# Kernel tuning notes

Hardware: AMD Instinct MI355X
Metric: run time of the kernel (lower is better)

## Reference

```python
import jax, jax.numpy as jnp
import numpy as np

D_MODEL = 512
D_FFN = 2048
N_LAYERS = 6
VOCAB = 1000
D_STATE = 16
D_CONV = 4
D_INNER = 2 * D_MODEL  # expand=2
DT_RANK = 32           # ceil(d_model/16)
B, LT, LS = 2, 512, 512


def _pos_encoding(length, d_model):
    pos = np.arange(length, dtype=np.float32)[:, None]
    div = np.exp(np.arange(0, d_model, 2, dtype=np.float32) * (-np.log(10000.0) / d_model))
    pe = np.zeros((length, d_model), np.float32)
    pe[:, 0::2] = np.sin(pos * div)
    pe[:, 1::2] = np.cos(pos * div)
    return jnp.asarray(pe)


def _layer_norm(x, g, b, eps=1e-6):
    m = x.mean(-1, keepdims=True)
    v = ((x - m) ** 2).mean(-1, keepdims=True)
    return (x - m) * jax.lax.rsqrt(v + eps) * g + b


def _mamba(x, in_w, conv_w, conv_b, xproj_w, dt_w, dt_b, A_log, Dskip, out_w):
    # x: (b, l, d_model)
    b, l, _ = x.shape
    xz = x @ in_w.T                                   # (b, l, 2*d_inner)
    xc, z = jnp.split(xz, 2, axis=-1)
    # causal depthwise conv over time
    xt = jnp.transpose(xc, (0, 2, 1))                 # (b, d_inner, l)
    xt = jnp.pad(xt, ((0, 0), (0, 0), (D_CONV - 1, 0)))
    xt = jax.lax.conv_general_dilated(
        xt, conv_w, window_strides=(1,), padding='VALID',
        feature_group_count=D_INNER, dimension_numbers=('NCH', 'OIH', 'NCH'))
    xc = jax.nn.silu(jnp.transpose(xt, (0, 2, 1)) + conv_b)  # (b, l, d_inner)
    dbl = xc @ xproj_w.T                              # (b, l, dt_rank + 2*n)
    dt, Bm, Cm = jnp.split(dbl, [DT_RANK, DT_RANK + D_STATE], axis=-1)
    dt = jax.nn.softplus(dt @ dt_w.T + dt_b)          # (b, l, d_inner)
    A = -jnp.exp(A_log)                               # (d_inner, n)

    def step(h, xs):
        dt_t, B_t, C_t, u_t = xs                      # (b,d),(b,n),(b,n),(b,d)
        dA = jnp.exp(dt_t[..., None] * A)             # (b, d, n)
        h = dA * h + (dt_t * u_t)[..., None] * B_t[:, None, :]
        y = jnp.einsum('bdn,bn->bd', h, C_t)
        return h, y

    h0 = jnp.zeros((b, D_INNER, D_STATE), x.dtype)
    xs = (jnp.swapaxes(dt, 0, 1), jnp.swapaxes(Bm, 0, 1),
          jnp.swapaxes(Cm, 0, 1), jnp.swapaxes(xc, 0, 1))
    _, ys = jax.lax.scan(step, h0, xs)                # ys: (l, b, d_inner)
    y = jnp.swapaxes(ys, 0, 1) + xc * Dskip
    y = y * jax.nn.silu(z)
    return y @ out_w.T                                # (b, l, d_model)


def setup_inputs() -> dict:
    key = jax.random.key(0)
    ks = iter(jax.random.split(key, 40))

    def rn(shape, s=0.02):
        return jax.random.normal(next(ks), shape, jnp.float32) * s

    def mamba_params():
        return dict(
            in_w=rn((N_LAYERS, 2 * D_INNER, D_MODEL)),
            conv_w=rn((N_LAYERS, D_INNER, 1, D_CONV), 0.1),
            conv_b=rn((N_LAYERS, D_INNER)),
            xproj=rn((N_LAYERS, DT_RANK + 2 * D_STATE, D_INNER)),
            dtw=rn((N_LAYERS, D_INNER, DT_RANK)),
            dtb=rn((N_LAYERS, D_INNER)),
            Alog=jnp.log(jnp.broadcast_to(jnp.arange(1.0, D_STATE + 1.0, dtype=jnp.float32), (N_LAYERS, D_INNER, D_STATE))),
            D=jnp.ones((N_LAYERS, D_INNER), jnp.float32),
            outw=rn((N_LAYERS, D_MODEL, D_INNER)),
        )

    ps, pc = mamba_params(), mamba_params()
    inp = {
        'src': jax.random.normal(next(ks), (B, LS, D_MODEL), jnp.float32),
        'tgt': jax.random.randint(next(ks), (B, LT), 0, VOCAB),
        'emb': rn((VOCAB, D_MODEL)),
        'in_w_s': ps['in_w'], 'conv_w_s': ps['conv_w'], 'conv_b_s': ps['conv_b'],
        'xproj_s': ps['xproj'], 'dtw_s': ps['dtw'], 'dtb_s': ps['dtb'],
        'Alog_s': ps['Alog'], 'D_s': ps['D'], 'outw_s': ps['outw'],
        'in_w_c': pc['in_w'], 'conv_w_c': pc['conv_w'], 'conv_b_c': pc['conv_b'],
        'xproj_c': pc['xproj'], 'dtw_c': pc['dtw'], 'dtb_c': pc['dtb'],
        'Alog_c': pc['Alog'], 'D_c': pc['D'], 'outw_c': pc['outw'],
        'ffn_w1': rn((N_LAYERS, D_FFN, D_MODEL)),
        'ffn_b1': jnp.zeros((N_LAYERS, D_FFN), jnp.float32),
        'ffn_w2': rn((N_LAYERS, D_MODEL, D_FFN)),
        'ffn_b2': jnp.zeros((N_LAYERS, D_MODEL), jnp.float32),
        'ln_g': jnp.ones((N_LAYERS, 3, D_MODEL), jnp.float32),
        'ln_b': jnp.zeros((N_LAYERS, 3, D_MODEL), jnp.float32),
        'fin_g': jnp.ones((D_MODEL,), jnp.float32),
        'fin_b': jnp.zeros((D_MODEL,), jnp.float32),
    }
    return inp


def reference(src, tgt, emb, in_w_s, conv_w_s, conv_b_s, xproj_s, dtw_s, dtb_s,
              Alog_s, D_s, outw_s, in_w_c, conv_w_c, conv_b_c, xproj_c, dtw_c,
              dtb_c, Alog_c, D_c, outw_c, ffn_w1, ffn_b1, ffn_w2, ffn_b2,
              ln_g, ln_b, fin_g, fin_b):
    # NormalizedEmbedding + sinusoidal positional encoding
    x = emb[tgt] * jnp.sqrt(jnp.asarray(D_MODEL, jnp.float32))
    x = x + _pos_encoding(LT, D_MODEL)[None]
    for i in range(N_LAYERS):
        # self mamba (post-norm, normalize_before=False)
        t2 = _mamba(x, in_w_s[i], conv_w_s[i], conv_b_s[i], xproj_s[i],
                    dtw_s[i], dtb_s[i], Alog_s[i], D_s[i], outw_s[i])
        x = _layer_norm(x + t2, ln_g[i, 0], ln_b[i, 0])
        # cross mamba over concat([memory, tgt]) then take last LT steps
        cat = jnp.concatenate([src, x], axis=1)
        t2 = _mamba(cat, in_w_c[i], conv_w_c[i], conv_b_c[i], xproj_c[i],
                    dtw_c[i], dtb_c[i], Alog_c[i], D_c[i], outw_c[i])[:, -LT:]
        x = _layer_norm(x + t2, ln_g[i, 1], ln_b[i, 1])
        # positionwise FFN
        h = jax.nn.relu(x @ ffn_w1[i].T + ffn_b1[i]) @ ffn_w2[i].T + ffn_b2[i]
        x = _layer_norm(x + h, ln_g[i, 2], ln_b[i, 2])
    return _layer_norm(x, fin_g, fin_b)
```

## Files before the change

kernel.cpp:

```cpp
#include <hip/hip_runtime.h>
#include <math.h>

#define DMODEL 512
#define DINNER 1024
#define DSTATE 16
#define DTRANK 32
#define NLAYERS 6
#define BB 2
#define LT 512
#define LS 512

typedef __attribute__((ext_vector_type(8))) short bf16x8;
typedef __attribute__((ext_vector_type(8))) unsigned short u16x8;
typedef __attribute__((ext_vector_type(4))) float f32x4;

__device__ __forceinline__ unsigned short f2bf(float f) {
  unsigned u = __float_as_uint(f);
  u += 0x7fffu + ((u >> 16) & 1u);
  return (unsigned short)(u >> 16);
}
__device__ __forceinline__ float bf2f(unsigned short u) {
  return __uint_as_float((unsigned)u << 16);
}

template<int EPI>
__device__ __forceinline__ float epi_apply(float acc, float b) {
  if (EPI == 1) { float v = acc + b; return v > 0.f ? v : 0.f; }
  if (EPI == 2) { return acc + b; }
  if (EPI == 3) { float v = acc + b; return fmaxf(v, 0.f) + log1pf(__expf(-fabsf(v))); }
  return acc;
}

__global__ __launch_bounds__(256) void cvt_all_kernel(
    const float* __restrict__ i0, const float* __restrict__ i1,
    const float* __restrict__ i2, const float* __restrict__ i3,
    const float* __restrict__ i4, const float* __restrict__ i5,
    const float* __restrict__ i6, const float* __restrict__ i7,
    const float* __restrict__ i8, const float* __restrict__ i9,
    unsigned short* __restrict__ outbase) {
  int i = blockIdx.x * 256 + threadIdx.x;
  if (i >= 8159232) return;
  const float* in; int off;
  if      (i < 1572864) { in = i0; off = i; }
  else if (i < 3145728) { in = i1; off = i - 1572864; }
  else if (i < 3244032) { in = i2; off = i - 3145728; }
  else if (i < 3342336) { in = i3; off = i - 3244032; }
  else if (i < 3391488) { in = i4; off = i - 3342336; }
  else if (i < 3440640) { in = i5; off = i - 3391488; }
  else if (i < 4227072) { in = i6; off = i - 3440640; }
  else if (i < 5013504) { in = i7; off = i - 4227072; }
  else if (i < 6586368) { in = i8; off = i - 5013504; }
  else                  { in = i9; off = i - 6586368; }
  float4 a = ((const float4*)in)[off];
  ushort4 o = make_ushort4(f2bf(a.x), f2bf(a.y), f2bf(a.z), f2bf(a.w));
  *(ushort4*)&outbase[(size_t)i * 4] = o;
}

__global__ __launch_bounds__(256) void embed_kernel(const int* __restrict__ tgt,
    const float* __restrict__ emb, float* __restrict__ X,
    unsigned short* __restrict__ Xb) {
  int i = blockIdx.x * 256 + threadIdx.x;
  int d = i & (DMODEL - 1);
  int bt = i >> 9;
  int t = bt & (LT - 1);
  int tok = tgt[bt];
  float div = __expf((float)(d & ~1) * (-9.210340371976184f / (float)DMODEL));
  float ang = (float)t * div;
  float pe = (d & 1) ? cosf(ang) : sinf(ang);
  float v = emb[(size_t)tok * DMODEL + d] * 22.627416997969522f + pe;
  X[i] = v;
  Xb[i] = f2bf(v);
}

__global__ __launch_bounds__(256) void catsrc_kernel(const float* __restrict__ src,
    unsigned short* __restrict__ CATb) {
  int i = blockIdx.x * 256 + threadIdx.x;
  int c8 = (i & 63) * 8;
  int r = i >> 6;
  int b = r >> 9, l = r & 511;
  const float* s = src + ((size_t)b * 512 + l) * DMODEL + c8;
  float4 a = *(const float4*)s;
  float4 bq = *(const float4*)(s + 4);
  u16x8 o;
  o[0] = f2bf(a.x); o[1] = f2bf(a.y); o[2] = f2bf(a.z); o[3] = f2bf(a.w);
  o[4] = f2bf(bq.x); o[5] = f2bf(bq.y); o[6] = f2bf(bq.z); o[7] = f2bf(bq.w);
  *(u16x8*)&CATb[((size_t)b * 1024 + l) * DMODEL + c8] = o;
}

template<int BK, int EPI, bool SPLIT, bool OUTB>
__global__ __launch_bounds__(256) void mgemmA(
    const unsigned short* __restrict__ A, const unsigned short* __restrict__ Bw,
    const float* __restrict__ bias, float* __restrict__ C,
    unsigned short* __restrict__ Cb, int M, int N, int K, int lda) {
  constexpr int PAD = BK + 8;
  constexpr int CHA = BK / 32;
  constexpr int CHB = BK / 16;
  __shared__ __align__(16) unsigned short As[64 * PAD];
  __shared__ __align__(16) unsigned short Bs[128 * PAD];
  const int tid = threadIdx.x;
  const int bn = blockIdx.x * 128;
  const int bm = blockIdx.y * 64;
  const int lane = tid & 63;
  const int w = tid >> 6;
  const int wr = (w >> 1) * 32;
  const int wc = (w & 1) * 64;
  const int l15 = lane & 15;
  const int l4 = lane >> 4;
  const int koff = l4 * 8;
  int kcnt = K, kbeg = 0;
  if (SPLIT) { kcnt = K / (int)gridDim.z; kbeg = blockIdx.z * kcnt; }
  const int nt = kcnt / BK;
  f32x4 acc[2][4] = {};

  int arow_[CHA], ak8_[CHA];
  const unsigned short* Ap[CHA];
#pragma unroll
  for (int i = 0; i < CHA; ++i) {
    int f = tid + 256 * i;
    arow_[i] = f / (BK / 8);
    ak8_[i] = (f % (BK / 8)) * 8;
    Ap[i] = A + (size_t)(bm + arow_[i]) * lda + kbeg + ak8_[i];
  }
  int brow_[CHB], bk8_[CHB];
  const unsigned short* Bp[CHB];
#pragma unroll
  for (int i = 0; i < CHB; ++i) {
    int f = tid + 256 * i;
    brow_[i] = f / (BK / 8);
    bk8_[i] = (f % (BK / 8)) * 8;
    Bp[i] = Bw + (size_t)(bn + brow_[i]) * K + kbeg + bk8_[i];
  }

  u16x8 av[CHA], bv[CHB];
#pragma unroll
  for (int i = 0; i < CHA; ++i) av[i] = *(const u16x8*)Ap[i];
#pragma unroll
  for (int i = 0; i < CHB; ++i) bv[i] = *(const u16x8*)Bp[i];

  for (int t = 0; t < nt; ++t) {
    __syncthreads();
#pragma unroll
    for (int i = 0; i < CHA; ++i) *(u16x8*)&As[arow_[i] * PAD + ak8_[i]] = av[i];
#pragma unroll
    for (int i = 0; i < CHB; ++i) *(u16x8*)&Bs[brow_[i] * PAD + bk8_[i]] = bv[i];
    if (t + 1 < nt) {
      int ko = (t + 1) * BK;
#pragma unroll
      for (int i = 0; i < CHA; ++i) av[i] = *(const u16x8*)(Ap[i] + ko);
#pragma unroll
      for (int i = 0; i < CHB; ++i) bv[i] = *(const u16x8*)(Bp[i] + ko);
    }
    __syncthreads();
#pragma unroll
    for (int kk = 0; kk < BK / 32; ++kk) {
      bf16x8 afr[2], bfr[4];
#pragma unroll
      for (int i = 0; i < 2; ++i)
        afr[i] = *(const bf16x8*)&As[(wr + i * 16 + l15) * PAD + kk * 32 + koff];
#pragma unroll
      for (int j = 0; j < 4; ++j)
        bfr[j] = *(const bf16x8*)&Bs[(wc + j * 16 + l15) * PAD + kk * 32 + koff];
#pragma unroll
      for (int fr = 0; fr < 2; ++fr)
#pragma unroll
        for (int fc = 0; fc < 4; ++fc)
          acc[fr][fc] = __builtin_amdgcn_mfma_f32_16x16x32_bf16(
              afr[fr], bfr[fc], acc[fr][fc], 0, 0, 0);
    }
  }

  if (SPLIT) {
    float* Pz = C + (size_t)blockIdx.z * M * N;
#pragma unroll
    for (int fc = 0; fc < 4; ++fc) {
      int col = bn + wc + fc * 16 + l15;
#pragma unroll
      for (int fr = 0; fr < 2; ++fr) {
        int row0 = bm + wr + fr * 16 + l4 * 4;
#pragma unroll
        for (int r = 0; r < 4; ++r)
          Pz[(size_t)(row0 + r) * N + col] = acc[fr][fc][r];
      }
    }
  } else {
#pragma unroll
    for (int fc = 0; fc < 4; ++fc) {
      int col = bn + wc + fc * 16 + l15;
      float bvs = (EPI != 0) ? bias[col] : 0.f;
#pragma unroll
      for (int fr = 0; fr < 2; ++fr) {
        int row0 = bm + wr + fr * 16 + l4 * 4;
#pragma unroll
        for (int r = 0; r < 4; ++r) {
          float v = epi_apply<EPI>(acc[fr][fc][r], bvs);
          if (OUTB) Cb[(size_t)(row0 + r) * N + col] = f2bf(v);
          else      C[(size_t)(row0 + r) * N + col] = v;
        }
      }
    }
  }
}

template<int BK, int EPI, bool SPLIT, bool OUTB>
__global__ __launch_bounds__(256) void mgemm(
    const unsigned short* __restrict__ A, const unsigned short* __restrict__ Bw,
    const float* __restrict__ bias, float* __restrict__ C,
    unsigned short* __restrict__ Cb, int M, int N, int K, int lda) {
  constexpr int PAD = BK + 8;
  constexpr int CH = BK / 32;
  __shared__ __align__(16) unsigned short As[64 * PAD];
  __shared__ __align__(16) unsigned short Bs[64 * PAD];
  const int tid = threadIdx.x;
  const int bn = blockIdx.x * 64;
  const int bm = blockIdx.y * 64;
  const int lane = tid & 63;
  const int w = tid >> 6;
  const int wr = (w >> 1) * 32;
  const int wc = (w & 1) * 32;
  const int l15 = lane & 15;
  const int l4 = lane >> 4;
  const int koff = l4 * 8;
  int kcnt = K, kbeg = 0;
  if (SPLIT) { kcnt = K / (int)gridDim.z; kbeg = blockIdx.z * kcnt; }
  const int nt = kcnt / BK;
  f32x4 acc[2][2] = {};

  int row_[CH], k8_[CH];
  const unsigned short *Ap[CH], *Bp[CH];
#pragma unroll
  for (int i = 0; i < CH; ++i) {
    int f = tid + 256 * i;
    row_[i] = f / (BK / 8);
    k8_[i] = (f % (BK / 8)) * 8;
    Ap[i] = A + (size_t)(bm + row_[i]) * lda + kbeg + k8_[i];
    Bp[i] = Bw + (size_t)(bn + row_[i]) * K + kbeg + k8_[i];
  }

  u16x8 av[CH], bv[CH];
#pragma unroll
  for (int i = 0; i < CH; ++i) { av[i] = *(const u16x8*)Ap[i]; bv[i] = *(const u16x8*)Bp[i]; }

  for (int t = 0; t < nt; ++t) {
    __syncthreads();
#pragma unroll
    for (int i = 0; i < CH; ++i) {
      *(u16x8*)&As[row_[i] * PAD + k8_[i]] = av[i];
      *(u16x8*)&Bs[row_[i] * PAD + k8_[i]] = bv[i];
    }
    if (t + 1 < nt) {
      int ko = (t + 1) * BK;
#pragma unroll
      for (int i = 0; i < CH; ++i) {
        av[i] = *(const u16x8*)(Ap[i] + ko);
        bv[i] = *(const u16x8*)(Bp[i] + ko);
      }
    }
    __syncthreads();
#pragma unroll
    for (int kk = 0; kk < CH; ++kk) {
      bf16x8 afr[2], bfr[2];
#pragma unroll
      for (int i = 0; i < 2; ++i) {
        afr[i] = *(const bf16x8*)&As[(wr + i * 16 + l15) * PAD + kk * 32 + koff];
        bfr[i] = *(const bf16x8*)&Bs[(wc + i * 16 + l15) * PAD + kk * 32 + koff];
      }
#pragma unroll
      for (int fr = 0; fr < 2; ++fr)
#pragma unroll
        for (int fc = 0; fc < 2; ++fc)
          acc[fr][fc] = __builtin_amdgcn_mfma_f32_16x16x32_bf16(
              afr[fr], bfr[fc], acc[fr][fc], 0, 0, 0);
    }
  }

  if (SPLIT) {
    float* Pz = C + (size_t)blockIdx.z * M * N;
#pragma unroll
    for (int fc = 0; fc < 2; ++fc) {
      int col = bn + wc + fc * 16 + l15;
#pragma unroll
      for (int fr = 0; fr < 2; ++fr) {
        int row0 = bm + wr + fr * 16 + l4 * 4;
#pragma unroll
        for (int r = 0; r < 4; ++r)
          Pz[(size_t)(row0 + r) * N + col] = acc[fr][fc][r];
      }
    }
  } else {
#pragma unroll
    for (int fc = 0; fc < 2; ++fc) {
      int col = bn + wc + fc * 16 + l15;
      float bvs = (EPI != 0) ? bias[col] : 0.f;
#pragma unroll
      for (int fr = 0; fr < 2; ++fr) {
        int row0 = bm + wr + fr * 16 + l4 * 4;
#pragma unroll
        for (int r = 0; r < 4; ++r) {
          float v = epi_apply<EPI>(acc[fr][fc][r], bvs);
          if (OUTB) Cb[(size_t)(row0 + r) * N + col] = f2bf(v);
          else      C[(size_t)(row0 + r) * N + col] = v;
        }
      }
    }
  }
}

__global__ __launch_bounds__(256) void mgemm_dt(
    const float* __restrict__ XPP, const unsigned short* __restrict__ Bw,
    const float* __restrict__ bias, unsigned short* __restrict__ Cb,
    int M, int N) {
  constexpr int PAD = 40;
  __shared__ __align__(16) unsigned short As[64 * PAD];
  __shared__ __align__(16) unsigned short Bs[64 * PAD];
  const int tid = threadIdx.x;
  const int bn = blockIdx.x * 64;
  const int bm = blockIdx.y * 64;
  const int lane = tid & 63;
  const int w = tid >> 6;
  const int wr = (w >> 1) * 32;
  const int wc = (w & 1) * 32;
  const int l15 = lane & 15;
  const int l4 = lane >> 4;
  const int koff = l4 * 8;
  const size_t zs = (size_t)M * 64;
  {
    int r = tid >> 2, c8 = (tid & 3) * 8;
    const float* p = XPP + (size_t)(bm + r) * 64 + c8;
    float s[8] = {0.f, 0.f, 0.f, 0.f, 0.f, 0.f, 0.f, 0.f};
#pragma unroll
    for (int z = 0; z < 8; ++z) {
      float4 a = *(const float4*)(p + z * zs);
      float4 b = *(const float4*)(p + z * zs + 4);
      s[0] += a.x; s[1] += a.y; s[2] += a.z; s[3] += a.w;
      s[4] += b.x; s[5] += b.y; s[6] += b.z; s[7] += b.w;
    }
    u16x8 o;
#pragma unroll
    for (int j = 0; j < 8; ++j) o[j] = f2bf(s[j]);
    *(u16x8*)&As[r * PAD + c8] = o;
    *(u16x8*)&Bs[r * PAD + c8] = *(const u16x8*)(Bw + (size_t)(bn + r) * 32 + c8);
  }
  __syncthreads();
  bf16x8 afr[2], bfr[2];
#pragma unroll
  for (int i = 0; i < 2; ++i) {
    afr[i] = *(const bf16x8*)&As[(wr + i * 16 + l15) * PAD + koff];
    bfr[i] = *(const bf16x8*)&Bs[(wc + i * 16 + l15) * PAD + koff];
  }
  f32x4 acc[2][2] = {};
#pragma unroll
  for (int fr = 0; fr < 2; ++fr)
#pragma unroll
    for (int fc = 0; fc < 2; ++fc)
      acc[fr][fc] = __builtin_amdgcn_mfma_f32_16x16x32_bf16(
          afr[fr], bfr[fc], acc[fr][fc], 0, 0, 0);
#pragma unroll
  for (int fc = 0; fc < 2; ++fc) {
    int col = bn + wc + fc * 16 + l15;
    float bvs = bias[col];
#pragma unroll
    for (int fr = 0; fr < 2; ++fr) {
      int row0 = bm + wr + fr * 16 + l4 * 4;
#pragma unroll
      for (int r = 0; r < 4; ++r)
        Cb[(size_t)(row0 + r) * N + col] = f2bf(epi_apply<3>(acc[fr][fc][r], bvs));
    }
  }
}

__global__ __launch_bounds__(256) void conv_silu_kernel(
    const unsigned short* __restrict__ xzb, const float* __restrict__ w,
    const float* __restrict__ bias, unsigned short* __restrict__ outb, int L) {
  int idx = blockIdx.x * 256 + threadIdx.x;
  int d8 = (idx & 127) * 8;
  int bt = idx >> 7;
  int b = bt / L;
  int t = bt - b * L;
  const unsigned short* col = xzb + ((size_t)b * L) * (2 * DINNER) + d8;
  float acc[8];
  float4 wv[8];
#pragma unroll
  for (int j = 0; j < 8; ++j) {
    acc[j] = bias[d8 + j];
    wv[j] = *(const float4*)(w + (size_t)(d8 + j) * 4);
  }
#pragma unroll
  for (int k = 0; k < 4; ++k) {
    int tt = t - 3 + k;
    if (tt >= 0) {
      u16x8 v = *(const u16x8*)(col + (size_t)tt * (2 * DINNER));
      float wk[8] = {
        k == 0 ? wv[0].x : k == 1 ? wv[0].y : k == 2 ? wv[0].z : wv[0].w,
        k == 0 ? wv[1].x : k == 1 ? wv[1].y : k == 2 ? wv[1].z : wv[1].w,
        k == 0 ? wv[2].x : k == 1 ? wv[2].y : k == 2 ? wv[2].z : wv[2].w,
        k == 0 ? wv[3].x : k == 1 ? wv[3].y : k == 2 ? wv[3].z : wv[3].w,
        k == 0 ? wv[4].x : k == 1 ? wv[4].y : k == 2 ? wv[4].z : wv[4].w,
        k == 0 ? wv[5].x : k == 1 ? wv[5].y : k == 2 ? wv[5].z : wv[5].w,
        k == 0 ? wv[6].x : k == 1 ? wv[6].y : k == 2 ? wv[6].z : wv[6].w,
        k == 0 ? wv[7].x : k == 1 ? wv[7].y : k == 2 ? wv[7].z : wv[7].w };
#pragma unroll
      for (int j = 0; j < 8; ++j) acc[j] = fmaf(bf2f(v[j]), wk[j], acc[j]);
    }
  }
  u16x8 o;
#pragma unroll
  for (int j = 0; j < 8; ++j) {
    float sig = 1.f / (1.f + __expf(-acc[j]));
    o[j] = f2bf(acc[j] * sig);
  }
  *(u16x8*)&outb[(size_t)bt * DINNER + d8] = o;
}

__global__ __launch_bounds__(256) void scan_pass1(
    const unsigned short* __restrict__ dt, const float* __restrict__ XPP,
    const unsigned short* __restrict__ u, const float* __restrict__ Alog,
    float* __restrict__ P, float* __restrict__ S, int L, int CL) {
  __shared__ float BC[32][32];
  const int tid = threadIdx.x;
  const int d = blockIdx.x * 256 + tid;
  const int b = blockIdx.y;
  const int c = blockIdx.z;
  const int t0 = c * CL;
  if (tid < CL * 4) {
    int t = tid >> 2, j8 = (tid & 3) * 8;
    const float* p = XPP + ((size_t)b * L + t0 + t) * 64 + 32 + j8;
    const size_t zs = (size_t)BB * L * 64;
    float s[8] = {0.f, 0.f, 0.f, 0.f, 0.f, 0.f, 0.f, 0.f};
#pragma unroll
    for (int z = 0; z < 8; ++z) {
      float4 a = *(const float4*)(p + z * zs);
      float4 bq = *(const float4*)(p + z * zs + 4);
      s[0] += a.x; s[1] += a.y; s[2] += a.z; s[3] += a.w;
      s[4] += bq.x; s[5] += bq.y; s[6] += bq.z; s[7] += bq.w;
    }
#pragma unroll
    for (int j = 0; j < 8; ++j) BC[t][j8 + j] = s[j];
  }
  float A[16], h[16], Pp[16];
#pragma unroll
  for (int j = 0; j < 4; ++j) {
    float4 a4 = *(const float4*)(Alog + d * 16 + j * 4);
    A[j * 4 + 0] = -__expf(a4.x); A[j * 4 + 1] = -__expf(a4.y);
    A[j * 4 + 2] = -__expf(a4.z); A[j * 4 + 3] = -__expf(a4.w);
  }
#pragma unroll
  for (int n = 0; n < 16; ++n) { h[n] = 0.f; Pp[n] = 1.f; }
  const unsigned short* dtp = dt + ((size_t)b * L + t0) * DINNER + d;
  const unsigned short* up  = u  + ((size_t)b * L + t0) * DINNER + d;
  __syncthreads();
  float dtv = bf2f(dtp[0]), uv = bf2f(up[0]);
  for (int t = 0; t < CL; ++t) {
    float dtn = 0.f, un = 0.f;
    if (t + 1 < CL) {
      dtn = bf2f(dtp[(size_t)(t + 1) * DINNER]);
      un  = bf2f(up[(size_t)(t + 1) * DINNER]);
    }
    float du = dtv * uv;
#pragma unroll
    for (int n = 0; n < 16; ++n) {
      float dA = __expf(dtv * A[n]);
      Pp[n] *= dA;
      h[n] = fmaf(dA, h[n], du * BC[t][n]);
    }
    dtv = dtn; uv = un;
  }
  size_t base = (size_t)c * 32768 + ((size_t)(b * 1024 + d) << 4);
#pragma unroll
  for (int j = 0; j < 4; ++j) {
    *(float4*)&P[base + j * 4] = make_float4(Pp[j*4], Pp[j*4+1], Pp[j*4+2], Pp[j*4+3]);
    *(float4*)&S[base + j * 4] = make_float4(h[j*4], h[j*4+1], h[j*4+2], h[j*4+3]);
  }
}

__global__ __launch_bounds__(256) void scan_pass2(
    const unsigned short* __restrict__ dt, const float* __restrict__ XPP,
    const unsigned short* __restrict__ u, const unsigned short* __restrict__ xzb,
    const float* __restrict__ Alog, const float* __restrict__ Dsk,
    const float* __restrict__ P, const float* __restrict__ S,
    unsigned short* __restrict__ ysb, int L, int CL, int c0) {
  __shared__ float BC[32][32];
  const int tid = threadIdx.x;
  const int d = blockIdx.x * 256 + tid;
  const int b = blockIdx.y;
  const int c = blockIdx.z + c0;
  const int t0 = c * CL;
  if (tid < CL * 4) {
    int t = tid >> 2, j8 = (tid & 3) * 8;
    const float* p = XPP + ((size_t)b * L + t0 + t) * 64 + 32 + j8;
    const size_t zs = (size_t)BB * L * 64;
    float s[8] = {0.f, 0.f, 0.f, 0.f, 0.f, 0.f, 0.f, 0.f};
#pragma unroll
    for (int z = 0; z < 8; ++z) {
      float4 a = *(const float4*)(p + z * zs);
      float4 bq = *(const float4*)(p + z * zs + 4);
      s[0] += a.x; s[1] += a.y; s[2] += a.z; s[3] += a.w;
      s[4] += bq.x; s[5] += bq.y; s[6] += bq.z; s[7] += bq.w;
    }
#pragma unroll
    for (int j = 0; j < 8; ++j) BC[t][j8 + j] = s[j];
  }
  float A[16], h[16];
#pragma unroll
  for (int j = 0; j < 4; ++j) {
    float4 a4 = *(const float4*)(Alog + d * 16 + j * 4);
    A[j * 4 + 0] = -__expf(a4.x); A[j * 4 + 1] = -__expf(a4.y);
    A[j * 4 + 2] = -__expf(a4.z); A[j * 4 + 3] = -__expf(a4.w);
  }
#pragma unroll
  for (int n = 0; n < 16; ++n) h[n] = 0.f;
  size_t sbase = (size_t)(b * 1024 + d) << 4;
  for (int cc = 0; cc < c; ++cc) {
    size_t bb = (size_t)cc * 32768 + sbase;
#pragma unroll
    for (int j = 0; j < 4; ++j) {
      float4 p4 = *(const float4*)&P[bb + j * 4];
      float4 s4 = *(const float4*)&S[bb + j * 4];
      h[j*4+0] = fmaf(p4.x, h[j*4+0], s4.x);
      h[j*4+1] = fmaf(p4.y, h[j*4+1], s4.y);
      h[j*4+2] = fmaf(p4.z, h[j*4+2], s4.z);
      h[j*4+3] = fmaf(p4.w, h[j*4+3], s4.w);
    }
  }
  float Dv = Dsk[d];
  const unsigned short* dtp = dt + ((size_t)b * L + t0) * DINNER + d;
  const unsigned short* up  = u  + ((size_t)b * L + t0) * DINNER + d;
  const unsigned short* zp  = xzb + ((size_t)b * L + t0) * (2 * DINNER) + DINNER + d;
  unsigned short* yp = ysb + ((size_t)(b * 512) + (t0 - c0 * CL)) * DINNER + d;
  __syncthreads();
  float dtv = bf2f(dtp[0]), uv = bf2f(up[0]), zv = bf2f(zp[0]);
  for (int t = 0; t < CL; ++t) {
    float dtn = 0.f, un = 0.f, zn = 0.f;
    if (t + 1 < CL) {
      dtn = bf2f(dtp[(size_t)(t + 1) * DINNER]);
      un  = bf2f(up[(size_t)(t + 1) * DINNER]);
      zn  = bf2f(zp[(size_t)(t + 1) * (2 * DINNER)]);
    }
    float du = dtv * uv;
    float y = 0.f;
#pragma unroll
    for (int n = 0; n < 16; ++n) {
      float dA = __expf(dtv * A[n]);
      h[n] = fmaf(dA, h[n], du * BC[t][n]);
      y = fmaf(h[n], BC[t][16 + n], y);
    }
    float sig = 1.f / (1.f + __expf(-zv));
    yp[(size_t)t * DINNER] = f2bf((y + uv * Dv) * (zv * sig));
    dtv = dtn; uv = un; zv = zn;
  }
}

template<int NZ, int EPI>
__global__ __launch_bounds__(64) void ln_red_kernel(
    const float* __restrict__ res, const float* __restrict__ P,
    const float* __restrict__ bias, const float* __restrict__ g,
    const float* __restrict__ be, float* __restrict__ out,
    unsigned short* __restrict__ outb, int row_scale, int row_off) {
  int r = blockIdx.x;
  int b = r >> 9, t = r & 511;
  int lane = threadIdx.x;
  const float* rp = res + (size_t)r * DMODEL;
  size_t ob = ((size_t)(b * row_scale + row_off + t)) * DMODEL;
  float v[8];
  float s = 0.f, ss = 0.f;
#pragma unroll
  for (int j = 0; j < 8; ++j) {
    int col = lane + j * 64;
    float acc = 0.f;
#pragma unroll
    for (int z = 0; z < NZ; ++z) acc += P[(size_t)z * 524288 + (size_t)r * DMODEL + col];
    float bv = (EPI != 0) ? bias[col] : 0.f;
    float x = rp[col] + epi_apply<EPI>(acc, bv);
    v[j] = x; s += x; ss += x * x;
  }
#pragma unroll
  for (int o = 32; o > 0; o >>= 1) { s += __shfl_xor(s, o); ss += __shfl_xor(ss, o); }
  float m = s * (1.f / 512.f);
  float var = ss * (1.f / 512.f) - m * m;
  float rs = rsqrtf(var + 1e-6f);
#pragma unroll
  for (int j = 0; j < 8; ++j) {
    int col = lane + j * 64;
    float o2 = (v[j] - m) * rs * g[col] + be[col];
    out[(size_t)r * DMODEL + col] = o2;
    outb[ob + col] = f2bf(o2);
  }
}

__global__ __launch_bounds__(64) void ln_final_kernel(
    const float* __restrict__ res, const float* __restrict__ g,
    const float* __restrict__ be, float* __restrict__ out) {
  int r = blockIdx.x;
  int lane = threadIdx.x;
  const float* rp = res + (size_t)r * DMODEL;
  float v[8];
  float s = 0.f, ss = 0.f;
#pragma unroll
  for (int j = 0; j < 8; ++j) {
    float x = rp[lane + j * 64];
    v[j] = x; s += x; ss += x * x;
  }
#pragma unroll
  for (int o = 32; o > 0; o >>= 1) { s += __shfl_xor(s, o); ss += __shfl_xor(ss, o); }
  float m = s * (1.f / 512.f);
  float var = ss * (1.f / 512.f) - m * m;
  float rs = rsqrtf(var + 1e-6f);
#pragma unroll
  for (int j = 0; j < 8; ++j) {
    int c = lane + j * 64;
    out[(size_t)r * DMODEL + c] = (v[j] - m) * rs * g[c] + be[c];
  }
}

extern "C" void kernel_launch(void* const* d_in, const int* in_sizes, int n_in,
                              void* d_out, int out_size, void* d_ws, size_t ws_size,
                              hipStream_t stream) {
  (void)in_sizes; (void)n_in; (void)out_size; (void)ws_size;
  const float* src      = (const float*)d_in[0];
  const int*   tgt      = (const int*)d_in[1];
  const float* emb      = (const float*)d_in[2];
  const float* in_w_s   = (const float*)d_in[3];
  const float* conv_w_s = (const float*)d_in[4];
  const float* conv_b_s = (const float*)d_in[5];
  const float* xproj_s  = (const float*)d_in[6];
  const float* dtw_s    = (const float*)d_in[7];
  const float* dtb_s    = (const float*)d_in[8];
  const float* Alog_s   = (const float*)d_in[9];
  const float* D_s      = (const float*)d_in[10];
  const float* outw_s   = (const float*)d_in[11];
  const float* in_w_c   = (const float*)d_in[12];
  const float* conv_w_c = (const float*)d_in[13];
  const float* conv_b_c = (const float*)d_in[14];
  const float* xproj_c  = (const float*)d_in[15];
  const float* dtw_c    = (const float*)d_in[16];
  const float* dtb_c    = (const float*)d_in[17];
  const float* Alog_c   = (const float*)d_in[18];
  const float* D_c      = (const float*)d_in[19];
  const float* outw_c   = (const float*)d_in[20];
  const float* ffn_w1   = (const float*)d_in[21];
  const float* ffn_b1   = (const float*)d_in[22];
  const float* ffn_w2   = (const float*)d_in[23];
  const float* ffn_b2   = (const float*)d_in[24];
  const float* ln_g     = (const float*)d_in[25];
  const float* ln_b     = (const float*)d_in[26];
  const float* fin_g    = (const float*)d_in[27];
  const float* fin_b    = (const float*)d_in[28];

  float* ws   = (float*)d_ws;
  float* X    = ws;
  float* XZ   = X + 524288;
  float* XPP  = XZ + 4194304;
  float* SC_P = XPP + 1048576;
  float* SC_S = SC_P + 1048576;
  unsigned short* U = (unsigned short*)(SC_S + 1048576);
  unsigned short* Xb   = U;
  unsigned short* CATb = Xb + 524288;
  unsigned short* XCb  = CATb + 1048576;
  unsigned short* XZb  = XCb + 2097152;
  unsigned short* YSb  = XZb + 4194304;
  unsigned short* DTb  = YSb + 1048576;
  unsigned short* WB   = DTb + 2097152;
  unsigned short* inwsb = WB;
  unsigned short* inwcb = inwsb + 6291456;
  unsigned short* xpsb  = inwcb + 6291456;
  unsigned short* xpcb  = xpsb + 393216;
  unsigned short* dtwsb = xpcb + 393216;
  unsigned short* dtwcb = dtwsb + 196608;
  unsigned short* owsb  = dtwcb + 196608;
  unsigned short* owcb  = owsb + 3145728;
  unsigned short* f1b   = owcb + 3145728;
  unsigned short* f2b   = f1b + 6291456;

  cvt_all_kernel<<<31872, 256, 0, stream>>>(
      in_w_s, in_w_c, xproj_s, xproj_c, dtw_s, dtw_c, outw_s, outw_c,
      ffn_w1, ffn_w2, WB);
  embed_kernel<<<2048, 256, 0, stream>>>(tgt, emb, X, Xb);
  catsrc_kernel<<<256, 256, 0, stream>>>(src, CATb);

  for (int i = 0; i < NLAYERS; ++i) {
    mgemm<64, 0, false, true><<<dim3(32, 16), 256, 0, stream>>>(
        Xb, inwsb + (size_t)i * 1048576, nullptr, nullptr, XZb, 1024, 2048, 512, 512);
    conv_silu_kernel<<<512, 256, 0, stream>>>(
        XZb, conv_w_s + (size_t)i * 4096, conv_b_s + (size_t)i * 1024, XCb, 512);
    mgemm<64, 0, true, false><<<dim3(1, 16, 8), 256, 0, stream>>>(
        XCb, xpsb + (size_t)i * 65536, nullptr, XPP, nullptr, 1024, 64, 1024, 1024);
    mgemm_dt<<<dim3(16, 16), 256, 0, stream>>>(
        XPP, dtwsb + (size_t)i * 32768, dtb_s + (size_t)i * 1024, DTb, 1024, 1024);
    scan_pass1<<<dim3(4, 2, 32), 256, 0, stream>>>(
        DTb, XPP, XCb, Alog_s + (size_t)i * 16384, SC_P, SC_S, 512, 16);
    scan_pass2<<<dim3(4, 2, 32), 256, 0, stream>>>(
        DTb, XPP, XCb, XZb, Alog_s + (size_t)i * 16384, D_s + (size_t)i * 1024,
        SC_P, SC_S, YSb, 512, 16, 0);
    mgemmA<64, 0, true, false><<<dim3(4, 16, 8), 256, 0, stream>>>(
        YSb, owsb + (size_t)i * 524288, nullptr, XZ, nullptr, 1024, 512, 1024, 1024);
    ln_red_kernel<8, 0><<<1024, 64, 0, stream>>>(
        X, XZ, nullptr, ln_g + (size_t)(i * 3 + 0) * 512,
        ln_b + (size_t)(i * 3 + 0) * 512, X, CATb, 1024, 512);

    mgemmA<64, 0, false, true><<<dim3(16, 32), 256, 0, stream>>>(
        CATb, inwcb + (size_t)i * 1048576, nullptr, nullptr, XZb, 2048, 2048, 512, 512);
    conv_silu_kernel<<<1024, 256, 0, stream>>>(
        XZb, conv_w_c + (size_t)i * 4096, conv_b_c + (size_t)i * 1024, XCb, 1024);
    mgemm<64, 0, true, false><<<dim3(1, 32, 8), 256, 0, stream>>>(
        XCb, xpcb + (size_t)i * 65536, nullptr, XPP, nullptr, 2048, 64, 1024, 1024);
    mgemm_dt<<<dim3(16, 32), 256, 0, stream>>>(
        XPP, dtwcb + (size_t)i * 32768, dtb_c + (size_t)i * 1024, DTb, 2048, 1024);
    scan_pass1<<<dim3(4, 2, 32), 256, 0, stream>>>(
        DTb, XPP, XCb, Alog_c + (size_t)i * 16384, SC_P, SC_S, 1024, 32);
    scan_pass2<<<dim3(4, 2, 16), 256, 0, stream>>>(
        DTb, XPP, XCb, XZb, Alog_c + (size_t)i * 16384, D_c + (size_t)i * 1024,
        SC_P, SC_S, YSb, 1024, 32, 16);
    mgemmA<64, 0, true, false><<<dim3(4, 16, 8), 256, 0, stream>>>(
        YSb, owcb + (size_t)i * 524288, nullptr, XZ, nullptr, 1024, 512, 1024, 1024);
    ln_red_kernel<8, 0><<<1024, 64, 0, stream>>>(
        X, XZ, nullptr, ln_g + (size_t)(i * 3 + 1) * 512,
        ln_b + (size_t)(i * 3 + 1) * 512, X, Xb, 512, 0);

    mgemm<64, 1, false, true><<<dim3(32, 16), 256, 0, stream>>>(
        Xb, f1b + (size_t)i * 1048576, ffn_b1 + (size_t)i * 2048, nullptr, XZb,
        1024, 2048, 512, 512);
    mgemmA<64, 0, true, false><<<dim3(4, 16, 8), 256, 0, stream>>>(
        XZb, f2b + (size_t)i * 1048576, nullptr, XZ, nullptr, 1024, 512, 2048, 2048);
    ln_red_kernel<8, 2><<<1024, 64, 0, stream>>>(
        X, XZ, ffn_b2 + (size_t)i * 512, ln_g + (size_t)(i * 3 + 2) * 512,
        ln_b + (size_t)(i * 3 + 2) * 512, X, Xb, 512, 0);
  }

  ln_final_kernel<<<1024, 64, 0, stream>>>(X, fin_g, fin_b, (float*)d_out);
}
```

Before: 1.216 ms.

## Fuse dt projection and softplus into scan passes; store split-K partials as bf16

Removes the separate dt-projection GEMM kernel and its bf16 DT buffer. Each scan thread now loads its 32 dt weights and bias, and recomputes dt from the reduced x_proj slice held in shared memory, in both scan passes. Split-K partial outputs of the out-projection and FFN2 GEMMs are written as bf16 instead of fp32 and summed in the layernorm-reduce kernel. This cuts launches and global memory traffic, in exchange for redundant dt arithmetic in both passes and lower precision in the partial sums.

```diff
diff --git a/kernel.cpp b/kernel.cpp
--- a/kernel.cpp
+++ b/kernel.cpp
@@ -170,7 +170,7 @@
   }
 
   if (SPLIT) {
-    float* Pz = C + (size_t)blockIdx.z * M * N;
+    unsigned short* Pz = Cb + (size_t)blockIdx.z * M * N;
 #pragma unroll
     for (int fc = 0; fc < 4; ++fc) {
       int col = bn + wc + fc * 16 + l15;
@@ -179,7 +179,7 @@
         int row0 = bm + wr + fr * 16 + l4 * 4;
 #pragma unroll
         for (int r = 0; r < 4; ++r)
-          Pz[(size_t)(row0 + r) * N + col] = acc[fr][fc][r];
+          Pz[(size_t)(row0 + r) * N + col] = f2bf(acc[fr][fc][r]);
       }
     }
   } else {
@@ -305,69 +305,6 @@
   }
 }
 
-__global__ __launch_bounds__(256) void mgemm_dt(
-    const float* __restrict__ XPP, const unsigned short* __restrict__ Bw,
-    const float* __restrict__ bias, unsigned short* __restrict__ Cb,
-    int M, int N) {
-  constexpr int PAD = 40;
-  __shared__ __align__(16) unsigned short As[64 * PAD];
-  __shared__ __align__(16) unsigned short Bs[64 * PAD];
-  const int tid = threadIdx.x;
-  const int bn = blockIdx.x * 64;
-  const int bm = blockIdx.y * 64;
-  const int lane = tid & 63;
-  const int w = tid >> 6;
-  const int wr = (w >> 1) * 32;
-  const int wc = (w & 1) * 32;
-  const int l15 = lane & 15;
-  const int l4 = lane >> 4;
-  const int koff = l4 * 8;
-  const size_t zs = (size_t)M * 64;
-  {
-    int r = tid >> 2, c8 = (tid & 3) * 8;
-    const float* p = XPP + (size_t)(bm + r) * 64 + c8;
-    float s[8] = {0.f, 0.f, 0.f, 0.f, 0.f, 0.f, 0.f, 0.f};
-#pragma unroll
-    for (int z = 0; z < 8; ++z) {
-      float4 a = *(const float4*)(p + z * zs);
-      float4 b = *(const float4*)(p + z * zs + 4);
-      s[0] += a.x; s[1] += a.y; s[2] += a.z; s[3] += a.w;
-      s[4] += b.x; s[5] += b.y; s[6] += b.z; s[7] += b.w;
-    }
-    u16x8 o;
-#pragma unroll
-    for (int j = 0; j < 8; ++j) o[j] = f2bf(s[j]);
-    *(u16x8*)&As[r * PAD + c8] = o;
-    *(u16x8*)&Bs[r * PAD + c8] = *(const u16x8*)(Bw + (size_t)(bn + r) * 32 + c8);
-  }
-  __syncthreads();
-  bf16x8 afr[2], bfr[2];
-#pragma unroll
-  for (int i = 0; i < 2; ++i) {
-    afr[i] = *(const bf16x8*)&As[(wr + i * 16 + l15) * PAD + koff];
-    bfr[i] = *(const bf16x8*)&Bs[(wc + i * 16 + l15) * PAD + koff];
-  }
-  f32x4 acc[2][2] = {};
-#pragma unroll
-  for (int fr = 0; fr < 2; ++fr)
-#pragma unroll
-    for (int fc = 0; fc < 2; ++fc)
-      acc[fr][fc] = __builtin_amdgcn_mfma_f32_16x16x32_bf16(
-          afr[fr], bfr[fc], acc[fr][fc], 0, 0, 0);
-#pragma unroll
-  for (int fc = 0; fc < 2; ++fc) {
-    int col = bn + wc + fc * 16 + l15;
-    float bvs = bias[col];
-#pragma unroll
-    for (int fr = 0; fr < 2; ++fr) {
-      int row0 = bm + wr + fr * 16 + l4 * 4;
-#pragma unroll
-      for (int r = 0; r < 4; ++r)
-        Cb[(size_t)(row0 + r) * N + col] = f2bf(epi_apply<3>(acc[fr][fc][r], bvs));
-    }
-  }
-}
-
 __global__ __launch_bounds__(256) void conv_silu_kernel(
     const unsigned short* __restrict__ xzb, const float* __restrict__ w,
     const float* __restrict__ bias, unsigned short* __restrict__ outb, int L) {
@@ -412,18 +349,19 @@
 }
 
 __global__ __launch_bounds__(256) void scan_pass1(
-    const unsigned short* __restrict__ dt, const float* __restrict__ XPP,
-    const unsigned short* __restrict__ u, const float* __restrict__ Alog,
-    float* __restrict__ P, float* __restrict__ S, int L, int CL) {
-  __shared__ float BC[32][32];
+    const float* __restrict__ XPP, const unsigned short* __restrict__ u,
+    const float* __restrict__ Alog, const float* __restrict__ dtw,
+    const float* __restrict__ dtb, float* __restrict__ P, float* __restrict__ S,
+    int L, int CL) {
+  __shared__ float DBL8[32][64];
   const int tid = threadIdx.x;
   const int d = blockIdx.x * 256 + tid;
   const int b = blockIdx.y;
   const int c = blockIdx.z;
   const int t0 = c * CL;
-  if (tid < CL * 4) {
-    int t = tid >> 2, j8 = (tid & 3) * 8;
-    const float* p = XPP + ((size_t)b * L + t0 + t) * 64 + 32 + j8;
+  if (tid < CL * 8) {
+    int t = tid >> 3, j8 = (tid & 7) * 8;
+    const float* p = XPP + ((size_t)b * L + t0 + t) * 64 + j8;
     const size_t zs = (size_t)BB * L * 64;
     float s[8] = {0.f, 0.f, 0.f, 0.f, 0.f, 0.f, 0.f, 0.f};
 #pragma unroll
@@ -434,35 +372,52 @@
       s[4] += bq.x; s[5] += bq.y; s[6] += bq.z; s[7] += bq.w;
     }
 #pragma unroll
-    for (int j = 0; j < 8; ++j) BC[t][j8 + j] = s[j];
-  }
-  float A[16], h[16], Pp[16];
+    for (int j = 0; j < 8; ++j) DBL8[t][j8 + j] = s[j];
+  }
+  float A[16];
 #pragma unroll
   for (int j = 0; j < 4; ++j) {
     float4 a4 = *(const float4*)(Alog + d * 16 + j * 4);
     A[j * 4 + 0] = -__expf(a4.x); A[j * 4 + 1] = -__expf(a4.y);
     A[j * 4 + 2] = -__expf(a4.z); A[j * 4 + 3] = -__expf(a4.w);
   }
+  float wreg[32];
+#pragma unroll
+  for (int j = 0; j < 8; ++j) {
+    float4 w4 = *(const float4*)(dtw + (size_t)d * 32 + j * 4);
+    wreg[j*4+0] = w4.x; wreg[j*4+1] = w4.y; wreg[j*4+2] = w4.z; wreg[j*4+3] = w4.w;
+  }
+  float dtbv = dtb[d];
+  float h[16], Pp[16];
 #pragma unroll
   for (int n = 0; n < 16; ++n) { h[n] = 0.f; Pp[n] = 1.f; }
-  const unsigned short* dtp = dt + ((size_t)b * L + t0) * DINNER + d;
-  const unsigned short* up  = u  + ((size_t)b * L + t0) * DINNER + d;
+  const unsigned short* up = u + ((size_t)b * L + t0) * DINNER + d;
   __syncthreads();
-  float dtv = bf2f(dtp[0]), uv = bf2f(up[0]);
   for (int t = 0; t < CL; ++t) {
-    float dtn = 0.f, un = 0.f;
-    if (t + 1 < CL) {
-      dtn = bf2f(dtp[(size_t)(t + 1) * DINNER]);
-      un  = bf2f(up[(size_t)(t + 1) * DINNER]);
-    }
+    float dtraw = dtbv;
+#pragma unroll
+    for (int k8 = 0; k8 < 8; ++k8) {
+      float4 q = *(const float4*)&DBL8[t][k8 * 4];
+      dtraw = fmaf(q.x, wreg[k8*4+0], dtraw);
+      dtraw = fmaf(q.y, wreg[k8*4+1], dtraw);
+      dtraw = fmaf(q.z, wreg[k8*4+2], dtraw);
+      dtraw = fmaf(q.w, wreg[k8*4+3], dtraw);
+    }
+    float dtv = fmaxf(dtraw, 0.f) + log1pf(__expf(-fabsf(dtraw)));
+    float uv = bf2f(up[(size_t)t * DINNER]);
     float du = dtv * uv;
+    float Bv[16];
+#pragma unroll
+    for (int j = 0; j < 4; ++j) {
+      float4 b4 = *(const float4*)&DBL8[t][32 + j * 4];
+      Bv[j*4+0] = b4.x; Bv[j*4+1] = b4.y; Bv[j*4+2] = b4.z; Bv[j*4+3] = b4.w;
+    }
 #pragma unroll
     for (int n = 0; n < 16; ++n) {
       float dA = __expf(dtv * A[n]);
       Pp[n] *= dA;
-      h[n] = fmaf(dA, h[n], du * BC[t][n]);
-    }
-    dtv = dtn; uv = un;
+      h[n] = fmaf(dA, h[n], du * Bv[n]);
+    }
   }
   size_t base = (size_t)c * 32768 + ((size_t)(b * 1024 + d) << 4);
 #pragma unroll
@@ -473,20 +428,21 @@
 }
 
 __global__ __launch_bounds__(256) void scan_pass2(
-    const unsigned short* __restrict__ dt, const float* __restrict__ XPP,
-    const unsigned short* __restrict__ u, const unsigned short* __restrict__ xzb,
-    const float* __restrict__ Alog, const float* __restrict__ Dsk,
-    const float* __restrict__ P, const float* __restrict__ S,
-    unsigned short* __restrict__ ysb, int L, int CL, int c0) {
-  __shared__ float BC[32][32];
+    const float* __restrict__ XPP, const unsigned short* __restrict__ u,
+    const unsigned short* __restrict__ xzb, const float* __restrict__ Alog,
+    const float* __restrict__ dtw, const float* __restrict__ dtb,
+    const float* __restrict__ Dsk, const float* __restrict__ P,
+    const float* __restrict__ S, unsigned short* __restrict__ ysb,
+    int L, int CL, int c0) {
+  __shared__ float DBL8[32][64];
   const int tid = threadIdx.x;
   const int d = blockIdx.x * 256 + tid;
   const int b = blockIdx.y;
   const int c = blockIdx.z + c0;
   const int t0 = c * CL;
-  if (tid < CL * 4) {
-    int t = tid >> 2, j8 = (tid & 3) * 8;
-    const float* p = XPP + ((size_t)b * L + t0 + t) * 64 + 32 + j8;
+  if (tid < CL * 8) {
+    int t = tid >> 3, j8 = (tid & 7) * 8;
+    const float* p = XPP + ((size_t)b * L + t0 + t) * 64 + j8;
     const size_t zs = (size_t)BB * L * 64;
     float s[8] = {0.f, 0.f, 0.f, 0.f, 0.f, 0.f, 0.f, 0.f};
 #pragma unroll
@@ -497,15 +453,23 @@
       s[4] += bq.x; s[5] += bq.y; s[6] += bq.z; s[7] += bq.w;
     }
 #pragma unroll
-    for (int j = 0; j < 8; ++j) BC[t][j8 + j] = s[j];
-  }
-  float A[16], h[16];
+    for (int j = 0; j < 8; ++j) DBL8[t][j8 + j] = s[j];
+  }
+  float A[16];
 #pragma unroll
   for (int j = 0; j < 4; ++j) {
     float4 a4 = *(const float4*)(Alog + d * 16 + j * 4);
     A[j * 4 + 0] = -__expf(a4.x); A[j * 4 + 1] = -__expf(a4.y);
     A[j * 4 + 2] = -__expf(a4.z); A[j * 4 + 3] = -__expf(a4.w);
   }
+  float wreg[32];
+#pragma unroll
+  for (int j = 0; j < 8; ++j) {
+    float4 w4 = *(const float4*)(dtw + (size_t)d * 32 + j * 4);
+    wreg[j*4+0] = w4.x; wreg[j*4+1] = w4.y; wreg[j*4+2] = w4.z; wreg[j*4+3] = w4.w;
+  }
+  float dtbv = dtb[d];
+  float h[16];
 #pragma unroll
   for (int n = 0; n < 16; ++n) h[n] = 0.f;
   size_t sbase = (size_t)(b * 1024 + d) << 4;
@@ -522,36 +486,47 @@
     }
   }
   float Dv = Dsk[d];
-  const unsigned short* dtp = dt + ((size_t)b * L + t0) * DINNER + d;
-  const unsigned short* up  = u  + ((size_t)b * L + t0) * DINNER + d;
-  const unsigned short* zp  = xzb + ((size_t)b * L + t0) * (2 * DINNER) + DINNER + d;
+  const unsigned short* up = u + ((size_t)b * L + t0) * DINNER + d;
+  const unsigned short* zp = xzb + ((size_t)b * L + t0) * (2 * DINNER) + DINNER + d;
   unsigned short* yp = ysb + ((size_t)(b * 512) + (t0 - c0 * CL)) * DINNER + d;
   __syncthreads();
-  float dtv = bf2f(dtp[0]), uv = bf2f(up[0]), zv = bf2f(zp[0]);
   for (int t = 0; t < CL; ++t) {
-    float dtn = 0.f, un = 0.f, zn = 0.f;
-    if (t + 1 < CL) {
-      dtn = bf2f(dtp[(size_t)(t + 1) * DINNER]);
-      un  = bf2f(up[(size_t)(t + 1) * DINNER]);
-      zn  = bf2f(zp[(size_t)(t + 1) * (2 * DINNER)]);
-    }
+    float dtraw = dtbv;
+#pragma unroll
+    for (int k8 = 0; k8 < 8; ++k8) {
+      float4 q = *(const float4*)&DBL8[t][k8 * 4];
+      dtraw = fmaf(q.x, wreg[k8*4+0], dtraw);
+      dtraw = fmaf(q.y, wreg[k8*4+1], dtraw);
+      dtraw = fmaf(q.z, wreg[k8*4+2], dtraw);
+      dtraw = fmaf(q.w, wreg[k8*4+3], dtraw);
+    }
+    float dtv = fmaxf(dtraw, 0.f) + log1pf(__expf(-fabsf(dtraw)));
+    float uv = bf2f(up[(size_t)t * DINNER]);
+    float zv = bf2f(zp[(size_t)t * (2 * DINNER)]);
     float du = dtv * uv;
+    float Bv[16], Cv[16];
+#pragma unroll
+    for (int j = 0; j < 4; ++j) {
+      float4 b4 = *(const float4*)&DBL8[t][32 + j * 4];
+      float4 c4 = *(const float4*)&DBL8[t][48 + j * 4];
+      Bv[j*4+0] = b4.x; Bv[j*4+1] = b4.y; Bv[j*4+2] = b4.z; Bv[j*4+3] = b4.w;
+      Cv[j*4+0] = c4.x; Cv[j*4+1] = c4.y; Cv[j*4+2] = c4.z; Cv[j*4+3] = c4.w;
+    }
     float y = 0.f;
 #pragma unroll
     for (int n = 0; n < 16; ++n) {
       float dA = __expf(dtv * A[n]);
-      h[n] = fmaf(dA, h[n], du * BC[t][n]);
-      y = fmaf(h[n], BC[t][16 + n], y);
+      h[n] = fmaf(dA, h[n], du * Bv[n]);
+      y = fmaf(h[n], Cv[n], y);
     }
     float sig = 1.f / (1.f + __expf(-zv));
     yp[(size_t)t * DINNER] = f2bf((y + uv * Dv) * (zv * sig));
-    dtv = dtn; uv = un; zv = zn;
   }
 }
 
 template<int NZ, int EPI>
 __global__ __launch_bounds__(64) void ln_red_kernel(
-    const float* __restrict__ res, const float* __restrict__ P,
+    const float* __restrict__ res, const unsigned short* __restrict__ Pb,
     const float* __restrict__ bias, const float* __restrict__ g,
     const float* __restrict__ be, float* __restrict__ out,
     unsigned short* __restrict__ outb, int row_scale, int row_off) {
@@ -567,7 +542,8 @@
     int col = lane + j * 64;
     float acc = 0.f;
 #pragma unroll
-    for (int z = 0; z < NZ; ++z) acc += P[(size_t)z * 524288 + (size_t)r * DMODEL + col];
+    for (int z = 0; z < NZ; ++z)
+      acc += bf2f(Pb[(size_t)z * 524288 + (size_t)r * DMODEL + col]);
     float bv = (EPI != 0) ? bias[col] : 0.f;
     float x = rp[col] + epi_apply<EPI>(acc, bv);
     v[j] = x; s += x; ss += x * x;
@@ -647,8 +623,7 @@
 
   float* ws   = (float*)d_ws;
   float* X    = ws;
-  float* XZ   = X + 524288;
-  float* XPP  = XZ + 4194304;
+  float* XPP  = X + 524288;
   float* SC_P = XPP + 1048576;
   float* SC_S = SC_P + 1048576;
   unsigned short* U = (unsigned short*)(SC_S + 1048576);
@@ -657,8 +632,8 @@
   unsigned short* XCb  = CATb + 1048576;
   unsigned short* XZb  = XCb + 2097152;
   unsigned short* YSb  = XZb + 4194304;
-  unsigned short* DTb  = YSb + 1048576;
-  unsigned short* WB   = DTb + 2097152;
+  unsigned short* XZPb = YSb + 1048576;
+  unsigned short* WB   = XZPb + 4194304;
   unsigned short* inwsb = WB;
   unsigned short* inwcb = inwsb + 6291456;
   unsigned short* xpsb  = inwcb + 6291456;
@@ -683,17 +658,16 @@
         XZb, conv_w_s + (size_t)i * 4096, conv_b_s + (size_t)i * 1024, XCb, 512);
     mgemm<64, 0, true, false><<<dim3(1, 16, 8), 256, 0, stream>>>(
         XCb, xpsb + (size_t)i * 65536, nullptr, XPP, nullptr, 1024, 64, 1024, 1024);
-    mgemm_dt<<<dim3(16, 16), 256, 0, stream>>>(
-        XPP, dtwsb + (size_t)i * 32768, dtb_s + (size_t)i * 1024, DTb, 1024, 1024);
     scan_pass1<<<dim3(4, 2, 32), 256, 0, stream>>>(
-        DTb, XPP, XCb, Alog_s + (size_t)i * 16384, SC_P, SC_S, 512, 16);
+        XPP, XCb, Alog_s + (size_t)i * 16384, dtw_s + (size_t)i * 32768,
+        dtb_s + (size_t)i * 1024, SC_P, SC_S, 512, 16);
     scan_pass2<<<dim3(4, 2, 32), 256, 0, stream>>>(
-        DTb, XPP, XCb, XZb, Alog_s + (size_t)i * 16384, D_s + (size_t)i * 1024,
-        SC_P, SC_S, YSb, 512, 16, 0);
+        XPP, XCb, XZb, Alog_s + (size_t)i * 16384, dtw_s + (size_t)i * 32768,
+        dtb_s + (size_t)i * 1024, D_s + (size_t)i * 1024, SC_P, SC_S, YSb, 512, 16, 0);
     mgemmA<64, 0, true, false><<<dim3(4, 16, 8), 256, 0, stream>>>(
-        YSb, owsb + (size_t)i * 524288, nullptr, XZ, nullptr, 1024, 512, 1024, 1024);
+        YSb, owsb + (size_t)i * 524288, nullptr, nullptr, XZPb, 1024, 512, 1024, 1024);
     ln_red_kernel<8, 0><<<1024, 64, 0, stream>>>(
-        X, XZ, nullptr, ln_g + (size_t)(i * 3 + 0) * 512,
+        X, XZPb, nullptr, ln_g + (size_t)(i * 3 + 0) * 512,
         ln_b + (size_t)(i * 3 + 0) * 512, X, CATb, 1024, 512);
 
     mgemmA<64, 0, false, true><<<dim3(16, 32), 256, 0, stream>>>(
@@ -702,26 +676,25 @@
         XZb, conv_w_c + (size_t)i * 4096, conv_b_c + (size_t)i * 1024, XCb, 1024);
     mgemm<64, 0, true, false><<<dim3(1, 32, 8), 256, 0, stream>>>(
         XCb, xpcb + (size_t)i * 65536, nullptr, XPP, nullptr, 2048, 64, 1024, 1024);
-    mgemm_dt<<<dim3(16, 32), 256, 0, stream>>>(
-        XPP, dtwcb + (size_t)i * 32768, dtb_c + (size_t)i * 1024, DTb, 2048, 1024);
     scan_pass1<<<dim3(4, 2, 32), 256, 0, stream>>>(
-        DTb, XPP, XCb, Alog_c + (size_t)i * 16384, SC_P, SC_S, 1024, 32);
+        XPP, XCb, Alog_c + (size_t)i * 16384, dtw_c + (size_t)i * 32768,
+        dtb_c + (size_t)i * 1024, SC_P, SC_S, 1024, 32);
     scan_pass2<<<dim3(4, 2, 16), 256, 0, stream>>>(
-        DTb, XPP, XCb, XZb, Alog_c + (size_t)i * 16384, D_c + (size_t)i * 1024,
-        SC_P, SC_S, YSb, 1024, 32, 16);
+        XPP, XCb, XZb, Alog_c + (size_t)i * 16384, dtw_c + (size_t)i * 32768,
+        dtb_c + (size_t)i * 1024, D_c + (size_t)i * 1024, SC_P, SC_S, YSb, 1024, 32, 16);
     mgemmA<64, 0, true, false><<<dim3(4, 16, 8), 256, 0, stream>>>(
-        YSb, owcb + (size_t)i * 524288, nullptr, XZ, nullptr, 1024, 512, 1024, 1024);
+        YSb, owcb + (size_t)i * 524288, nullptr, nullptr, XZPb, 1024, 512, 1024, 1024);
     ln_red_kernel<8, 0><<<1024, 64, 0, stream>>>(
-        X, XZ, nullptr, ln_g + (size_t)(i * 3 + 1) * 512,
+        X, XZPb, nullptr, ln_g + (size_t)(i * 3 + 1) * 512,
         ln_b + (size_t)(i * 3 + 1) * 512, X, Xb, 512, 0);
 
     mgemm<64, 1, false, true><<<dim3(32, 16), 256, 0, stream>>>(
         Xb, f1b + (size_t)i * 1048576, ffn_b1 + (size_t)i * 2048, nullptr, XZb,
         1024, 2048, 512, 512);
     mgemmA<64, 0, true, false><<<dim3(4, 16, 8), 256, 0, stream>>>(
-        XZb, f2b + (size_t)i * 1048576, nullptr, XZ, nullptr, 1024, 512, 2048, 2048);
+        XZb, f2b + (size_t)i * 1048576, nullptr, nullptr, XZPb, 1024, 512, 2048, 2048);
     ln_red_kernel<8, 2><<<1024, 64, 0, stream>>>(
-        X, XZ, ffn_b2 + (size_t)i * 512, ln_g + (size_t)(i * 3 + 2) * 512,
+        X, XZPb, ffn_b2 + (size_t)i * 512, ln_g + (size_t)(i * 3 + 2) * 512,
         ln_b + (size_t)(i * 3 + 2) * 512, X, Xb, 512, 0);
   }
 
```

After: 1.135 ms. 1.07x faster.
